# Kernel optimization log

Measured on AMD Instinct MI355X. Metric: run time of the kernel, lower is better.

## Reference

```python
import jax, jax.numpy as jnp
import numpy as np

B, S, H, I, E = 2, 2048, 1024, 2048, 8
TOP_K = 2

def setup_inputs() -> dict:
    key = jax.random.key(0)
    k1, k2, k3, k4 = jax.random.split(key, 4)
    hidden_states = jax.random.normal(k1, (B, S, H), dtype=jnp.float32)
    # gate initialized xavier_uniform with gain=0.1 -> small weights
    gate_w = jax.random.normal(k2, (E, H), dtype=jnp.float32) * 0.02
    w_up = jax.random.normal(k3, (E, H, I), dtype=jnp.float32) * 0.02
    w_down = jax.random.normal(k4, (E, I, H), dtype=jnp.float32) * 0.02
    return {"hidden_states": hidden_states, "gate_w": gate_w, "w_up": w_up, "w_down": w_down}

def reference(hidden_states, gate_w, w_up, w_down):
    b, s, h = hidden_states.shape
    e = gate_w.shape[0]
    x = hidden_states.reshape(-1, h)            # [T, H]
    T = x.shape[0]

    # --- Router (eval mode: no jitter noise) ---
    logits = x @ gate_w.T                       # [T, E]
    probs = jax.nn.softmax(logits, axis=-1)
    weights, idx = jax.lax.top_k(probs, TOP_K)  # [T, K]
    weights = weights / (weights.sum(axis=-1, keepdims=True) + 1e-9)

    # Combine weights as a [T, E] scatter of the normalized top-k probs
    combine = jnp.zeros((T, e), dtype=x.dtype)
    combine = combine.at[jnp.arange(T)[:, None], idx].add(weights)

    # --- Expert FFN (silu), computed for all experts then weighted-combined ---
    hmid = jax.nn.silu(jnp.einsum('th,ehi->tei', x, w_up))   # [T, E, I]
    y = jnp.einsum('tei,eih->teh', hmid, w_down)             # [T, E, H]
    out = jnp.einsum('te,teh->th', combine, y)               # [T, H]
    return out.reshape(b, s, h)
```

## Files before the change

### kernel.cpp

```cpp
#include <hip/hip_runtime.h>
#include <math.h>

#define T_TOK 4096
#define H_DIM 1024
#define I_DIM 2048
#define E_NUM 8
#define CAP   2048
#define BM 128
#define BN 128
#define BK 64

typedef __attribute__((ext_vector_type(8))) short bf16x8;
typedef __attribute__((ext_vector_type(4))) float f32x4;

__device__ __forceinline__ unsigned short f2bf(float f) {
    union { float f; unsigned int u; } v; v.f = f;
    unsigned int r = v.u + 0x7FFFu + ((v.u >> 16) & 1u);
    return (unsigned short)(r >> 16);
}

__device__ __forceinline__ void gl_lds16(const void* g, void* l) {
    __builtin_amdgcn_global_load_lds(
        (const __attribute__((address_space(1))) void*)g,
        (__attribute__((address_space(3))) void*)l, 16, 0, 0);
}

__global__ __launch_bounds__(256) void moe_router(
    const float* __restrict__ x, const float* __restrict__ gate,
    int* __restrict__ topk_idx, float* __restrict__ topk_w)
{
    const int wave = threadIdx.x >> 6;
    const int lane = threadIdx.x & 63;
    const int t = blockIdx.x * 4 + wave;

    float acc[E_NUM];
#pragma unroll
    for (int e = 0; e < E_NUM; ++e) acc[e] = 0.f;
    const float* xp = x + (size_t)t * H_DIM;
    for (int k = lane; k < H_DIM; k += 64) {
        const float xv = xp[k];
#pragma unroll
        for (int e = 0; e < E_NUM; ++e) acc[e] += xv * gate[e * H_DIM + k];
    }
#pragma unroll
    for (int e = 0; e < E_NUM; ++e) {
#pragma unroll
        for (int off = 32; off > 0; off >>= 1)
            acc[e] += __shfl_xor(acc[e], off, 64);
    }
    if (lane == 0) {
        float m = acc[0];
#pragma unroll
        for (int e = 1; e < E_NUM; ++e) m = fmaxf(m, acc[e]);
        float p[E_NUM]; float Z = 0.f;
#pragma unroll
        for (int e = 0; e < E_NUM; ++e) { p[e] = expf(acc[e] - m); Z += p[e]; }
        const float invZ = 1.f / Z;
        int i1 = 0, i2 = 0; float v1 = -1.f, v2 = -1.f;
#pragma unroll
        for (int e = 0; e < E_NUM; ++e) {
            const float pe = p[e] * invZ;
            if (pe > v1)      { v2 = v1; i2 = i1; v1 = pe; i1 = e; }
            else if (pe > v2) { v2 = pe; i2 = e; }
        }
        const float s = 1.f / (v1 + v2 + 1e-9f);
        topk_idx[t * 2 + 0] = i1; topk_idx[t * 2 + 1] = i2;
        topk_w[t * 2 + 0] = v1 * s; topk_w[t * 2 + 1] = v2 * s;
    }
}

__global__ __launch_bounds__(256) void moe_build(
    const int* __restrict__ topk_idx, const float* __restrict__ topk_w,
    int* __restrict__ counts, int* __restrict__ list_tok, float* __restrict__ list_w)
{
    const int e = blockIdx.x;
    const int tid = threadIdx.x;
    const int wv = tid >> 6, lane = tid & 63;
    __shared__ int wsum[4];
    int base = 0;
    for (int c = 0; c < T_TOK; c += 256) {
        const int t = c + tid;
        const int i0 = topk_idx[t * 2 + 0];
        const int i1 = topk_idx[t * 2 + 1];
        const int match = (i0 == e) || (i1 == e);
        const float w = (i0 == e) ? topk_w[t * 2 + 0] : topk_w[t * 2 + 1];
        const unsigned long long mask = __ballot(match);
        const int my = __popcll(mask & ((1ull << lane) - 1ull));
        if (lane == 0) wsum[wv] = __popcll(mask);
        __syncthreads();
        int woff = 0;
#pragma unroll
        for (int i = 0; i < 4; ++i) if (i < wv) woff += wsum[i];
        const int ctot = wsum[0] + wsum[1] + wsum[2] + wsum[3];
        if (match) {
            const int pos = base + woff + my;
            if (pos < CAP) { list_tok[e * CAP + pos] = t; list_w[e * CAP + pos] = w; }
        }
        base += ctot;
        __syncthreads();
    }
    if (tid == 0) counts[e] = min(base, CAP);
}

__global__ __launch_bounds__(256) void moe_gather(
    const float* __restrict__ x, const int* __restrict__ counts,
    const int* __restrict__ list_tok, unsigned short* __restrict__ Xg)
{
    const int e = blockIdx.y;
    const int r = blockIdx.x;
    if (r >= min(counts[e], CAP)) return;
    const int tok = list_tok[e * CAP + r];
    const float4 v = ((const float4*)(x + (size_t)tok * H_DIM))[threadIdx.x];
    ushort4 o = make_ushort4(f2bf(v.x), f2bf(v.y), f2bf(v.z), f2bf(v.w));
    *(ushort4*)(Xg + (size_t)(e * CAP + r) * H_DIM + threadIdx.x * 4) = o;
}

__global__ __launch_bounds__(256) void transpose_bf16(
    const float* __restrict__ in, unsigned short* __restrict__ outp, int R, int C)
{
    __shared__ unsigned short t[64][72];
    const int e = blockIdx.z;
    const float* src = in + (size_t)e * R * C;
    unsigned short* dst = outp + (size_t)e * R * C;
    const int c0 = blockIdx.x * 64;
    const int r0 = blockIdx.y * 64;
    const int tx = (threadIdx.x & 15) << 2;
    const int ty = threadIdx.x >> 4;
#pragma unroll
    for (int s = 0; s < 4; ++s) {
        const int r = ty + s * 16;
        const float4 v = *(const float4*)&src[(size_t)(r0 + r) * C + c0 + tx];
        t[tx + 0][r] = f2bf(v.x);
        t[tx + 1][r] = f2bf(v.y);
        t[tx + 2][r] = f2bf(v.z);
        t[tx + 3][r] = f2bf(v.w);
    }
    __syncthreads();
    const int cc = threadIdx.x >> 3;
    const int rr = (threadIdx.x & 7) << 3;
#pragma unroll
    for (int s = 0; s < 2; ++s) {
        const int c = cc + s * 32;
        *(bf16x8*)&dst[(size_t)(c0 + c) * R + r0 + rr] = *(const bf16x8*)&t[c][rr];
    }
}


__global__ __launch_bounds__(256) void moe_gemm1(
    const unsigned short* __restrict__ Xg, const unsigned short* __restrict__ WupT,
    const int* __restrict__ counts, unsigned short* __restrict__ hmid)
{
    __shared__ unsigned short As[2][BM][BK];
    __shared__ unsigned short Bs[2][BN][BK];
    const int s_id = blockIdx.x;
    const int l = (s_id & 7) * 256 + (s_id >> 3);
    const int e = l >> 8;
    const int bx = l & 15;
    const int by = (l >> 4) & 15;
    const int cnt = min(counts[e], CAP);
    const int row0 = bx * BM;
    if (row0 >= cnt) return;
    const int n0 = by * BN;
    const int tid = threadIdx.x;
    const int lane = tid & 63;
    const int wid = tid >> 6;
    const int wm = wid >> 1, wn = wid & 1;

    const unsigned short* Ae = Xg + (size_t)e * CAP * H_DIM;
    const unsigned short* Be = WupT + (size_t)e * (size_t)I_DIM * H_DIM;

    const int sub = lane >> 3;
    const int kus = ((lane & 7) ^ sub) * 8;

#define STAGE1(buf, kt)                                                       \
    {                                                                         \
        _Pragma("unroll")                                                     \
        for (int c = 0; c < 4; ++c) {                                         \
            const int row = (c * 4 + wid) * 8 + sub;                          \
            gl_lds16(Ae + (size_t)(row0 + row) * H_DIM + (kt) + kus,          \
                     (char*)&As[buf][0][0] + (c * 4 + wid) * 1024);           \
            gl_lds16(Be + (size_t)(n0 + row) * H_DIM + (kt) + kus,            \
                     (char*)&Bs[buf][0][0] + (c * 4 + wid) * 1024);           \
        }                                                                     \
    }

    f32x4 acc[4][4];
#pragma unroll
    for (int m = 0; m < 4; ++m)
#pragma unroll
        for (int n = 0; n < 4; ++n) acc[m][n] = (f32x4){0.f, 0.f, 0.f, 0.f};

    STAGE1(0, 0);
    __syncthreads();
    int cur = 0;
    for (int kt = 0; kt < H_DIM; kt += BK) {
        if (kt + BK < H_DIM) STAGE1(cur ^ 1, kt + BK);
#pragma unroll
        for (int kk = 0; kk < BK; kk += 32) {
            const int koff = ((((kk >> 3) | (lane >> 4)) ^ (lane & 7)) << 3);
            bf16x8 a[4], b[4];
#pragma unroll
            for (int m = 0; m < 4; ++m)
                a[m] = *(const bf16x8*)&As[cur][wm * 64 + m * 16 + (lane & 15)][koff];
#pragma unroll
            for (int n = 0; n < 4; ++n)
                b[n] = *(const bf16x8*)&Bs[cur][wn * 64 + n * 16 + (lane & 15)][koff];
#pragma unroll
            for (int m = 0; m < 4; ++m)
#pragma unroll
                for (int n = 0; n < 4; ++n)
                    acc[m][n] = __builtin_amdgcn_mfma_f32_16x16x32_bf16(
                        a[m], b[n], acc[m][n], 0, 0, 0);
        }
        __syncthreads();
        cur ^= 1;
    }
#undef STAGE1

    unsigned short* He = hmid + (size_t)e * CAP * I_DIM;
#pragma unroll
    for (int m = 0; m < 4; ++m) {
        const int rb = row0 + wm * 64 + m * 16 + ((lane >> 4) << 2);
#pragma unroll
        for (int n = 0; n < 4; ++n) {
            const int col = n0 + wn * 64 + n * 16 + (lane & 15);
#pragma unroll
            for (int j = 0; j < 4; ++j) {
                const float v = acc[m][n][j];
                const float s = v / (1.f + __expf(-v));
                He[(size_t)(rb + j) * I_DIM + col] = f2bf(s);
            }
        }
    }
}

__global__ __launch_bounds__(256) void moe_gemm2(
    const unsigned short* __restrict__ hmid, const unsigned short* __restrict__ WdownT,
    const int* __restrict__ counts, const int* __restrict__ list_tok,
    const float* __restrict__ list_w, float* __restrict__ out)
{
    __shared__ unsigned short As[2][BM][BK];
    __shared__ unsigned short Bs[2][BN][BK];
    const int s_id = blockIdx.x;
    const int l = (s_id & 7) * 256 + (s_id >> 3);
    const int e = l >> 8;
    const int bx = l & 15;
    const int by = (l >> 4) & 7;
    const int kh = (l >> 7) & 1;
    const int cnt = min(counts[e], CAP);
    const int row0 = bx * BM;
    if (row0 >= cnt) return;
    const int n0 = by * BN;
    const int kbase = kh * (I_DIM / 2);
    const int tid = threadIdx.x;
    const int lane = tid & 63;
    const int wid = tid >> 6;
    const int wm = wid >> 1, wn = wid & 1;

    const unsigned short* Ae = hmid + (size_t)e * CAP * I_DIM;
    const unsigned short* Be = WdownT + (size_t)e * (size_t)H_DIM * I_DIM;

    const int sub = lane >> 3;
    const int kus = ((lane & 7) ^ sub) * 8;

#define STAGE2(buf, kt)                                                       \
    {                                                                         \
        _Pragma("unroll")                                                     \
        for (int c = 0; c < 4; ++c) {                                         \
            const int row = (c * 4 + wid) * 8 + sub;                          \
            gl_lds16(Ae + (size_t)(row0 + row) * I_DIM + kbase + (kt) + kus,  \
                     (char*)&As[buf][0][0] + (c * 4 + wid) * 1024);           \
            gl_lds16(Be + (size_t)(n0 + row) * I_DIM + kbase + (kt) + kus,    \
                     (char*)&Bs[buf][0][0] + (c * 4 + wid) * 1024);           \
        }                                                                     \
    }

    f32x4 acc[4][4];
#pragma unroll
    for (int m = 0; m < 4; ++m)
#pragma unroll
        for (int n = 0; n < 4; ++n) acc[m][n] = (f32x4){0.f, 0.f, 0.f, 0.f};

    STAGE2(0, 0);
    __syncthreads();
    int cur = 0;
    for (int kt = 0; kt < I_DIM / 2; kt += BK) {
        if (kt + BK < I_DIM / 2) STAGE2(cur ^ 1, kt + BK);
#pragma unroll
        for (int kk = 0; kk < BK; kk += 32) {
            const int koff = ((((kk >> 3) | (lane >> 4)) ^ (lane & 7)) << 3);
            bf16x8 a[4], b[4];
#pragma unroll
            for (int m = 0; m < 4; ++m)
                a[m] = *(const bf16x8*)&As[cur][wm * 64 + m * 16 + (lane & 15)][koff];
#pragma unroll
            for (int n = 0; n < 4; ++n)
                b[n] = *(const bf16x8*)&Bs[cur][wn * 64 + n * 16 + (lane & 15)][koff];
#pragma unroll
            for (int m = 0; m < 4; ++m)
#pragma unroll
                for (int n = 0; n < 4; ++n)
                    acc[m][n] = __builtin_amdgcn_mfma_f32_16x16x32_bf16(
                        a[m], b[n], acc[m][n], 0, 0, 0);
        }
        __syncthreads();
        cur ^= 1;
    }
#undef STAGE2

#pragma unroll
    for (int m = 0; m < 4; ++m) {
#pragma unroll
        for (int j = 0; j < 4; ++j) {
            const int gr = row0 + wm * 64 + m * 16 + ((lane >> 4) << 2) + j;
            if (gr < cnt) {
                const int tok = list_tok[e * CAP + gr];
                const float w = list_w[e * CAP + gr];
                float* op = out + (size_t)tok * H_DIM + n0 + wn * 64 + (lane & 15);
#pragma unroll
                for (int n = 0; n < 4; ++n)
                    atomicAdd(op + n * 16, w * acc[m][n][j]);
            }
        }
    }
}

extern "C" void kernel_launch(void* const* d_in, const int* in_sizes, int n_in,
                              void* d_out, int out_size, void* d_ws, size_t ws_size,
                              hipStream_t stream)
{
    const float* x      = (const float*)d_in[0];
    const float* gate   = (const float*)d_in[1];
    const float* w_up   = (const float*)d_in[2];
    const float* w_down = (const float*)d_in[3];
    float* out = (float*)d_out;

    char* ws = (char*)d_ws;
    int*   counts   = (int*)(ws);
    int*   topk_idx = (int*)(ws + 1024);
    float* topk_w   = (float*)(ws + 33792);
    int*   list_tok = (int*)(ws + 66560);
    float* list_w   = (float*)(ws + 132096);
    unsigned short* Xg     = (unsigned short*)(ws + 197632);
    unsigned short* WupT   = (unsigned short*)(ws + 197632 + 33554432ull);
    unsigned short* WdownT = (unsigned short*)(ws + 197632 + 67108864ull);
    unsigned short* hmid   = (unsigned short*)(ws + 197632 + 100663296ull);

    hipMemsetAsync(out, 0, (size_t)out_size * sizeof(float), stream);

    moe_router<<<T_TOK / 4, 256, 0, stream>>>(x, gate, topk_idx, topk_w);
    moe_build<<<E_NUM, 256, 0, stream>>>(topk_idx, topk_w, counts, list_tok, list_w);
    moe_gather<<<dim3(CAP, E_NUM), 256, 0, stream>>>(x, counts, list_tok, Xg);
    transpose_bf16<<<dim3(I_DIM / 64, H_DIM / 64, E_NUM), 256, 0, stream>>>(w_up, WupT, H_DIM, I_DIM);
    transpose_bf16<<<dim3(H_DIM / 64, I_DIM / 64, E_NUM), 256, 0, stream>>>(w_down, WdownT, I_DIM, H_DIM);
    moe_gemm1<<<2048, 256, 0, stream>>>(Xg, WupT, counts, hmid);
    moe_gemm2<<<2048, 256, 0, stream>>>(hmid, WdownT, counts, list_tok, list_w, out);
}
```

Before: 369.3 us.

## Replace atomic split-K scatter with bf16 expert outputs and a gather-combine kernel

GEMM2 no longer splits K in halves or atomically adds weighted results into the output. It writes per-expert bf16 rows into a reused workspace buffer, and a new combine kernel gathers each token's two expert rows through a position map built in moe_build. This removes the output memset and the float atomics, at the cost of one extra launch and a bf16 rounding of the expert outputs. Both GEMM main loops also swap __syncthreads for explicit vmcnt waits plus raw barriers so the prefetch of the next tile can stay in flight during compute.

```diff
diff --git a/kernel.cpp b/kernel.cpp
--- a/kernel.cpp
+++ b/kernel.cpp
@@ -18,6 +18,10 @@
     unsigned int r = v.u + 0x7FFFu + ((v.u >> 16) & 1u);
     return (unsigned short)(r >> 16);
 }
+__device__ __forceinline__ float bf2f(unsigned short u) {
+    union { unsigned int u; float f; } v; v.u = (unsigned int)u << 16;
+    return v.f;
+}
 
 __device__ __forceinline__ void gl_lds16(const void* g, void* l) {
     __builtin_amdgcn_global_load_lds(
@@ -70,8 +74,8 @@
 }
 
 __global__ __launch_bounds__(256) void moe_build(
-    const int* __restrict__ topk_idx, const float* __restrict__ topk_w,
-    int* __restrict__ counts, int* __restrict__ list_tok, float* __restrict__ list_w)
+    const int* __restrict__ topk_idx, int* __restrict__ counts,
+    int* __restrict__ list_tok, int* __restrict__ pos_arr)
 {
     const int e = blockIdx.x;
     const int tid = threadIdx.x;
@@ -83,7 +87,7 @@
         const int i0 = topk_idx[t * 2 + 0];
         const int i1 = topk_idx[t * 2 + 1];
         const int match = (i0 == e) || (i1 == e);
-        const float w = (i0 == e) ? topk_w[t * 2 + 0] : topk_w[t * 2 + 1];
+        const int slot = (i0 == e) ? 0 : 1;
         const unsigned long long mask = __ballot(match);
         const int my = __popcll(mask & ((1ull << lane) - 1ull));
         if (lane == 0) wsum[wv] = __popcll(mask);
@@ -94,7 +98,10 @@
         const int ctot = wsum[0] + wsum[1] + wsum[2] + wsum[3];
         if (match) {
             const int pos = base + woff + my;
-            if (pos < CAP) { list_tok[e * CAP + pos] = t; list_w[e * CAP + pos] = w; }
+            if (pos < CAP) {
+                list_tok[e * CAP + pos] = t;
+                pos_arr[t * 2 + slot] = e * CAP + pos;
+            }
         }
         base += ctot;
         __syncthreads();
@@ -191,10 +198,18 @@
         for (int n = 0; n < 4; ++n) acc[m][n] = (f32x4){0.f, 0.f, 0.f, 0.f};
 
     STAGE1(0, 0);
-    __syncthreads();
+    asm volatile("s_waitcnt vmcnt(0)" ::: "memory");
+    __builtin_amdgcn_s_barrier();
     int cur = 0;
     for (int kt = 0; kt < H_DIM; kt += BK) {
-        if (kt + BK < H_DIM) STAGE1(cur ^ 1, kt + BK);
+        if (kt + BK < H_DIM) {
+            STAGE1(cur ^ 1, kt + BK);
+            asm volatile("s_waitcnt vmcnt(8)" ::: "memory");
+        } else {
+            asm volatile("s_waitcnt vmcnt(0)" ::: "memory");
+        }
+        __builtin_amdgcn_s_barrier();
+        __builtin_amdgcn_sched_barrier(0);
 #pragma unroll
         for (int kk = 0; kk < BK; kk += 32) {
             const int koff = ((((kk >> 3) | (lane >> 4)) ^ (lane & 7)) << 3);
@@ -212,7 +227,7 @@
                     acc[m][n] = __builtin_amdgcn_mfma_f32_16x16x32_bf16(
                         a[m], b[n], acc[m][n], 0, 0, 0);
         }
-        __syncthreads();
+        __builtin_amdgcn_s_barrier();
         cur ^= 1;
     }
 #undef STAGE1
@@ -236,22 +251,19 @@
 
 __global__ __launch_bounds__(256) void moe_gemm2(
     const unsigned short* __restrict__ hmid, const unsigned short* __restrict__ WdownT,
-    const int* __restrict__ counts, const int* __restrict__ list_tok,
-    const float* __restrict__ list_w, float* __restrict__ out)
+    const int* __restrict__ counts, unsigned short* __restrict__ y)
 {
     __shared__ unsigned short As[2][BM][BK];
     __shared__ unsigned short Bs[2][BN][BK];
     const int s_id = blockIdx.x;
-    const int l = (s_id & 7) * 256 + (s_id >> 3);
-    const int e = l >> 8;
+    const int l = (s_id & 7) * 128 + (s_id >> 3);
+    const int e = l >> 7;
     const int bx = l & 15;
     const int by = (l >> 4) & 7;
-    const int kh = (l >> 7) & 1;
     const int cnt = min(counts[e], CAP);
     const int row0 = bx * BM;
     if (row0 >= cnt) return;
     const int n0 = by * BN;
-    const int kbase = kh * (I_DIM / 2);
     const int tid = threadIdx.x;
     const int lane = tid & 63;
     const int wid = tid >> 6;
@@ -268,9 +280,9 @@
         _Pragma("unroll")                                                     \
         for (int c = 0; c < 4; ++c) {                                         \
             const int row = (c * 4 + wid) * 8 + sub;                          \
-            gl_lds16(Ae + (size_t)(row0 + row) * I_DIM + kbase + (kt) + kus,  \
+            gl_lds16(Ae + (size_t)(row0 + row) * I_DIM + (kt) + kus,          \
                      (char*)&As[buf][0][0] + (c * 4 + wid) * 1024);           \
-            gl_lds16(Be + (size_t)(n0 + row) * I_DIM + kbase + (kt) + kus,    \
+            gl_lds16(Be + (size_t)(n0 + row) * I_DIM + (kt) + kus,            \
                      (char*)&Bs[buf][0][0] + (c * 4 + wid) * 1024);           \
         }                                                                     \
     }
@@ -282,10 +294,18 @@
         for (int n = 0; n < 4; ++n) acc[m][n] = (f32x4){0.f, 0.f, 0.f, 0.f};
 
     STAGE2(0, 0);
-    __syncthreads();
+    asm volatile("s_waitcnt vmcnt(0)" ::: "memory");
+    __builtin_amdgcn_s_barrier();
     int cur = 0;
-    for (int kt = 0; kt < I_DIM / 2; kt += BK) {
-        if (kt + BK < I_DIM / 2) STAGE2(cur ^ 1, kt + BK);
+    for (int kt = 0; kt < I_DIM; kt += BK) {
+        if (kt + BK < I_DIM) {
+            STAGE2(cur ^ 1, kt + BK);
+            asm volatile("s_waitcnt vmcnt(8)" ::: "memory");
+        } else {
+            asm volatile("s_waitcnt vmcnt(0)" ::: "memory");
+        }
+        __builtin_amdgcn_s_barrier();
+        __builtin_amdgcn_sched_barrier(0);
 #pragma unroll
         for (int kk = 0; kk < BK; kk += 32) {
             const int koff = ((((kk >> 3) | (lane >> 4)) ^ (lane & 7)) << 3);
@@ -303,26 +323,46 @@
                     acc[m][n] = __builtin_amdgcn_mfma_f32_16x16x32_bf16(
                         a[m], b[n], acc[m][n], 0, 0, 0);
         }
-        __syncthreads();
+        __builtin_amdgcn_s_barrier();
         cur ^= 1;
     }
 #undef STAGE2
 
+    unsigned short* Ye = y + (size_t)e * CAP * H_DIM;
 #pragma unroll
     for (int m = 0; m < 4; ++m) {
 #pragma unroll
         for (int j = 0; j < 4; ++j) {
             const int gr = row0 + wm * 64 + m * 16 + ((lane >> 4) << 2) + j;
             if (gr < cnt) {
-                const int tok = list_tok[e * CAP + gr];
-                const float w = list_w[e * CAP + gr];
-                float* op = out + (size_t)tok * H_DIM + n0 + wn * 64 + (lane & 15);
-#pragma unroll
-                for (int n = 0; n < 4; ++n)
-                    atomicAdd(op + n * 16, w * acc[m][n][j]);
+#pragma unroll
+                for (int n = 0; n < 4; ++n) {
+                    const int col = n0 + wn * 64 + n * 16 + (lane & 15);
+                    Ye[(size_t)gr * H_DIM + col] = f2bf(acc[m][n][j]);
+                }
             }
         }
     }
+}
+
+__global__ __launch_bounds__(256) void moe_combine(
+    const unsigned short* __restrict__ y, const int* __restrict__ pos_arr,
+    const float* __restrict__ topk_w, float* __restrict__ out)
+{
+    const int t = blockIdx.x;
+    const int p0 = pos_arr[t * 2 + 0];
+    const int p1 = pos_arr[t * 2 + 1];
+    const float w0 = topk_w[t * 2 + 0];
+    const float w1 = topk_w[t * 2 + 1];
+    const int h = threadIdx.x * 4;
+    const ushort4 a = *(const ushort4*)&y[(size_t)p0 * H_DIM + h];
+    const ushort4 b = *(const ushort4*)&y[(size_t)p1 * H_DIM + h];
+    float4 o;
+    o.x = w0 * bf2f(a.x) + w1 * bf2f(b.x);
+    o.y = w0 * bf2f(a.y) + w1 * bf2f(b.y);
+    o.z = w0 * bf2f(a.z) + w1 * bf2f(b.z);
+    o.w = w0 * bf2f(a.w) + w1 * bf2f(b.w);
+    *(float4*)&out[(size_t)t * H_DIM + h] = o;
 }
 
 extern "C" void kernel_launch(void* const* d_in, const int* in_sizes, int n_in,
@@ -340,19 +380,19 @@
     int*   topk_idx = (int*)(ws + 1024);
     float* topk_w   = (float*)(ws + 33792);
     int*   list_tok = (int*)(ws + 66560);
-    float* list_w   = (float*)(ws + 132096);
+    int*   pos_arr  = (int*)(ws + 132096);
     unsigned short* Xg     = (unsigned short*)(ws + 197632);
     unsigned short* WupT   = (unsigned short*)(ws + 197632 + 33554432ull);
     unsigned short* WdownT = (unsigned short*)(ws + 197632 + 67108864ull);
     unsigned short* hmid   = (unsigned short*)(ws + 197632 + 100663296ull);
-
-    hipMemsetAsync(out, 0, (size_t)out_size * sizeof(float), stream);
+    unsigned short* y      = Xg;
 
     moe_router<<<T_TOK / 4, 256, 0, stream>>>(x, gate, topk_idx, topk_w);
-    moe_build<<<E_NUM, 256, 0, stream>>>(topk_idx, topk_w, counts, list_tok, list_w);
+    moe_build<<<E_NUM, 256, 0, stream>>>(topk_idx, counts, list_tok, pos_arr);
     moe_gather<<<dim3(CAP, E_NUM), 256, 0, stream>>>(x, counts, list_tok, Xg);
     transpose_bf16<<<dim3(I_DIM / 64, H_DIM / 64, E_NUM), 256, 0, stream>>>(w_up, WupT, H_DIM, I_DIM);
     transpose_bf16<<<dim3(H_DIM / 64, I_DIM / 64, E_NUM), 256, 0, stream>>>(w_down, WdownT, I_DIM, H_DIM);
     moe_gemm1<<<2048, 256, 0, stream>>>(Xg, WupT, counts, hmid);
-    moe_gemm2<<<2048, 256, 0, stream>>>(hmid, WdownT, counts, list_tok, list_w, out);
-}
+    moe_gemm2<<<1024, 256, 0, stream>>>(hmid, WdownT, counts, y);
+    moe_combine<<<T_TOK, 256, 0, stream>>>(y, pos_arr, topk_w, out);
+}
```

New measurement: 345.0 us. 6.6% less time.
